# Kernel tuning notes

Measured on AMD Instinct MI355X. Metric: run time of the kernel, lower is better.

Reference implementation:

```python
import jax, jax.numpy as jnp
import numpy as np

N = 150000   # nodes
E = 600000   # edges
F_IN = 32    # node features
H = 128      # hidden_channels == MLP_neurons
G = 2048     # graphs in batch


def setup_inputs() -> dict:
    key = jax.random.key(0)
    ks = iter(jax.random.split(key, 40))
    inp = {}
    inp['x'] = jax.random.normal(next(ks), (N, F_IN), dtype=jnp.float32)
    inp['edge_index'] = jax.random.randint(next(ks), (2, E), 0, N)
    inp['batch'] = jnp.sort(jax.random.randint(next(ks), (N,), 0, G))
    # GINConv MLPs: Linear(in,H) ReLU Linear(H,H) ReLU Linear(H,H)
    for i, f_in in enumerate([F_IN, H, H]):
        s1 = 1.0 / np.sqrt(f_in)
        s2 = 1.0 / np.sqrt(H)
        inp[f'c{i}_w1'] = jax.random.uniform(next(ks), (f_in, H), minval=-s1, maxval=s1)
        inp[f'c{i}_b1'] = jnp.zeros((H,), jnp.float32)
        inp[f'c{i}_w2'] = jax.random.uniform(next(ks), (H, H), minval=-s2, maxval=s2)
        inp[f'c{i}_b2'] = jnp.zeros((H,), jnp.float32)
        inp[f'c{i}_w3'] = jax.random.uniform(next(ks), (H, H), minval=-s2, maxval=s2)
        inp[f'c{i}_b3'] = jnp.zeros((H,), jnp.float32)
    s = 1.0 / np.sqrt(H)
    inp['fc0_w'] = jax.random.uniform(next(ks), (H, H), minval=-s, maxval=s)
    inp['fc0_b'] = jnp.zeros((H,), jnp.float32)
    inp['fc1_w'] = jax.random.uniform(next(ks), (H, H), minval=-s, maxval=s)
    inp['fc1_b'] = jnp.zeros((H,), jnp.float32)
    inp['out_w'] = jax.random.uniform(next(ks), (H, 2), minval=-s, maxval=s)
    inp['out_b'] = jnp.zeros((2,), jnp.float32)
    return inp


def _gin_layer(x, edge_index, w1, b1, w2, b2, w3, b3):
    # GINConv with eps=0: h = MLP(x + sum_{j in N(i)} x_j)
    agg = jax.ops.segment_sum(x[edge_index[0]], edge_index[1], num_segments=N)
    h = x + agg
    h = jax.nn.relu(h @ w1 + b1)
    h = jax.nn.relu(h @ w2 + b2)
    h = h @ w3 + b3
    return jax.nn.relu(h)  # outer .relu() in forward


def reference(x, edge_index, batch,
              c0_w1, c0_b1, c0_w2, c0_b2, c0_w3, c0_b3,
              c1_w1, c1_b1, c1_w2, c1_b2, c1_w3, c1_b3,
              c2_w1, c2_b1, c2_w2, c2_b2, c2_w3, c2_b3,
              fc0_w, fc0_b, fc1_w, fc1_b, out_w, out_b):
    h = _gin_layer(x, edge_index, c0_w1, c0_b1, c0_w2, c0_b2, c0_w3, c0_b3)
    h = _gin_layer(h, edge_index, c1_w1, c1_b1, c1_w2, c1_b2, c1_w3, c1_b3)
    h = _gin_layer(h, edge_index, c2_w1, c2_b1, c2_w2, c2_b2, c2_w3, c2_b3)
    # global_mean_pool over graph ids
    sums = jax.ops.segment_sum(h, batch, num_segments=G)            # [G,H]
    cnts = jax.ops.segment_sum(jnp.ones((N,), h.dtype), batch, num_segments=G)
    g = sums / jnp.maximum(cnts, 1.0)[:, None]
    # classifier head (dropout is identity at inference)
    g = jax.nn.relu(g @ fc0_w + fc0_b)
    g = jax.nn.relu(g @ fc1_w + fc1_b)
    return g @ out_w + out_b  # [G,2]
```

## Files before the change

kernel.cpp:

```cpp
#include <hip/hip_runtime.h>
#include <hip/hip_bf16.h>

#define NN 150000
#define EE 600000
#define F_IN 32
#define HD 128
#define GG 2048
#define CAP 28
#define NP 150016

typedef __attribute__((ext_vector_type(8))) short bf16x8;
typedef __attribute__((ext_vector_type(4))) float f32x4;

__device__ inline void split_bf16(float v, unsigned short& hi, unsigned short& lo) {
    __hip_bfloat16 h = __float2bfloat16(v);
    float hv = __bfloat162float(h);
    __hip_bfloat16 l = __float2bfloat16(v - hv);
    hi = *reinterpret_cast<unsigned short*>(&h);
    lo = *reinterpret_cast<unsigned short*>(&l);
}
__device__ inline unsigned short bf16_hi(float v) {
    __hip_bfloat16 h = __float2bfloat16(v);
    return *reinterpret_cast<unsigned short*>(&h);
}
__device__ inline float bf2f(unsigned short u) {
    union { unsigned int i; float f; } c;
    c.i = ((unsigned int)u) << 16;
    return c.f;
}

__global__ void init_zero(int* __restrict__ cnt_node, float* __restrict__ pooled) {
    int i = blockIdx.x * blockDim.x + threadIdx.x;
    if (i < NN) cnt_node[i] = 0;
    if (i < GG * HD) pooled[i] = 0.f;
}

__global__ void build_graph(const int* __restrict__ ei,
                            int* __restrict__ cnt_node,
                            int* __restrict__ bucket) {
    int e = blockIdx.x * blockDim.x + threadIdx.x;
    if (e >= EE) return;
    int src = ei[e];
    int dst = ei[EE + e];
    int slot = atomicAdd(&cnt_node[dst], 1);
    if (slot < CAP) bucket[dst * CAP + slot] = src;
}

struct PrepDesc { const float* src; unsigned short* dhi; unsigned short* dlo; int K; };
struct PrepArgs { PrepDesc d[9]; };

__global__ void prep_weights(PrepArgs pa) {
    PrepDesc de = pa.d[blockIdx.y];
    int total = de.K * HD;
    int KS = de.K >> 5;
    for (int idx = blockIdx.x * blockDim.x + threadIdx.x; idx < total;
         idx += gridDim.x * blockDim.x) {
        int k = idx / HD, h = idx - (idx / HD) * HD;
        unsigned short hi, lo;
        split_bf16(de.src[idx], hi, lo);
        int nt = h >> 4, m = h & 15;
        int ks = k >> 5, quad = (k >> 3) & 3, e = k & 7;
        int lane = quad * 16 + m;
        int pidx = ((nt * KS + ks) * 64 + lane) * 8 + e;
        de.dhi[pidx] = hi;
        de.dlo[pidx] = lo;
    }
}

template <int K_IN, bool BF16IN, bool POOL>
__launch_bounds__(256, 3)
__global__ void gin_layer(const void* __restrict__ hin_,
                          const int* __restrict__ cnt_node,
                          const int* __restrict__ bucket,
                          const unsigned short* __restrict__ w1h, const unsigned short* __restrict__ w1l,
                          const float* __restrict__ b1,
                          const unsigned short* __restrict__ w2h, const unsigned short* __restrict__ w2l,
                          const float* __restrict__ b2,
                          const unsigned short* __restrict__ w3h, const unsigned short* __restrict__ w3l,
                          const float* __restrict__ b3,
                          unsigned short* __restrict__ out,
                          const int* __restrict__ batch,
                          float* __restrict__ pooled) {
    constexpr int KS1 = K_IN / 32;
    constexpr int UN = BF16IN ? 4 : (KS1 == 1 ? 8 : 2);
    __shared__ unsigned int shp[4][16][128];

    const int wave = threadIdx.x >> 6;
    const int lane = threadIdx.x & 63;
    const int m = lane & 15;
    const int quad = lane >> 4;
    const int nodeBase = blockIdx.x * 128 + wave * 32;

    const float* hf = (const float*)hin_;
    const unsigned short* hb = (const unsigned short*)hin_;

    bf16x8 ah[2][KS1], al[2][KS1];
#pragma unroll
    for (int s = 0; s < 2; s++) {
        int node = nodeBase + s * 16 + m;
        node = node < NN ? node : NN - 1;
        float ag[KS1][8];
        if (BF16IN) {
            const unsigned short* rs = hb + (size_t)node * K_IN + quad * 8;
#pragma unroll
            for (int ks = 0; ks < KS1; ks++) {
                bf16x8 v = *(const bf16x8*)(rs + ks * 32);
#pragma unroll
                for (int e = 0; e < 8; e++) ag[ks][e] = bf2f((unsigned short)v[e]);
            }
        } else {
            const float* rs = hf + (size_t)node * K_IN + quad * 8;
#pragma unroll
            for (int ks = 0; ks < KS1; ks++) {
                float4 v0 = *(const float4*)(rs + ks * 32);
                float4 v1 = *(const float4*)(rs + ks * 32 + 4);
                ag[ks][0] = v0.x; ag[ks][1] = v0.y; ag[ks][2] = v0.z; ag[ks][3] = v0.w;
                ag[ks][4] = v1.x; ag[ks][5] = v1.y; ag[ks][6] = v1.z; ag[ks][7] = v1.w;
            }
        }
        int cnt = cnt_node[node];
        cnt = cnt < CAP ? cnt : CAP;
        const int* b = bucket + (size_t)node * CAP;
        int i = 0;
        if (BF16IN) {
            for (; i + UN <= cnt; i += UN) {
                bf16x8 v[UN][KS1];
#pragma unroll
                for (int j = 0; j < UN; j++) {
                    const unsigned short* r = hb + (size_t)b[i + j] * K_IN + quad * 8;
#pragma unroll
                    for (int ks = 0; ks < KS1; ks++)
                        v[j][ks] = *(const bf16x8*)(r + ks * 32);
                }
#pragma unroll
                for (int ks = 0; ks < KS1; ks++)
#pragma unroll
                    for (int e = 0; e < 8; e++) {
                        float t01 = bf2f((unsigned short)v[0][ks][e]) +
                                    bf2f((unsigned short)v[1][ks][e]);
                        float t23 = bf2f((unsigned short)v[2][ks][e]) +
                                    bf2f((unsigned short)v[3][ks][e]);
                        ag[ks][e] += t01 + t23;
                    }
            }
            for (; i < cnt; i++) {
                const unsigned short* r = hb + (size_t)b[i] * K_IN + quad * 8;
#pragma unroll
                for (int ks = 0; ks < KS1; ks++) {
                    bf16x8 v = *(const bf16x8*)(r + ks * 32);
#pragma unroll
                    for (int e = 0; e < 8; e++) ag[ks][e] += bf2f((unsigned short)v[e]);
                }
            }
        } else {
            for (; i + UN <= cnt; i += UN) {
                float4 v0[UN][KS1], v1[UN][KS1];
#pragma unroll
                for (int j = 0; j < UN; j++) {
                    const float* r = hf + (size_t)b[i + j] * K_IN + quad * 8;
#pragma unroll
                    for (int ks = 0; ks < KS1; ks++) {
                        v0[j][ks] = *(const float4*)(r + ks * 32);
                        v1[j][ks] = *(const float4*)(r + ks * 32 + 4);
                    }
                }
#pragma unroll
                for (int ks = 0; ks < KS1; ks++) {
#pragma unroll
                    for (int e = 0; e < 4; e++) {
                        float s01 = (&v0[0][ks].x)[e] + (&v0[1][ks].x)[e];
                        float s23 = (&v0[2][ks].x)[e] + (&v0[3][ks].x)[e];
                        if (UN == 8) {
                            s01 += (&v0[4][ks].x)[e] + (&v0[5][ks].x)[e];
                            s23 += (&v0[6][ks].x)[e] + (&v0[7][ks].x)[e];
                        }
                        ag[ks][e] += s01 + s23;
                    }
#pragma unroll
                    for (int e = 0; e < 4; e++) {
                        float s01 = (&v1[0][ks].x)[e] + (&v1[1][ks].x)[e];
                        float s23 = (&v1[2][ks].x)[e] + (&v1[3][ks].x)[e];
                        if (UN == 8) {
                            s01 += (&v1[4][ks].x)[e] + (&v1[5][ks].x)[e];
                            s23 += (&v1[6][ks].x)[e] + (&v1[7][ks].x)[e];
                        }
                        ag[ks][e + 4] += s01 + s23;
                    }
                }
            }
            for (; i < cnt; i++) {
                const float* r = hf + (size_t)b[i] * K_IN + quad * 8;
#pragma unroll
                for (int ks = 0; ks < KS1; ks++) {
                    float4 v0 = *(const float4*)(r + ks * 32);
                    float4 v1 = *(const float4*)(r + ks * 32 + 4);
                    ag[ks][0] += v0.x; ag[ks][1] += v0.y; ag[ks][2] += v0.z; ag[ks][3] += v0.w;
                    ag[ks][4] += v1.x; ag[ks][5] += v1.y; ag[ks][6] += v1.z; ag[ks][7] += v1.w;
                }
            }
        }
#pragma unroll
        for (int ks = 0; ks < KS1; ks++) {
            bf16x8 vh, vl;
#pragma unroll
            for (int e = 0; e < 8; e++) {
                unsigned short hi, lo;
                split_bf16(ag[ks][e], hi, lo);
                vh[e] = (short)hi;
                vl[e] = (short)lo;
            }
            ah[s][ks] = vh;
            al[s][ks] = vl;
        }
    }

    bf16x8 a2h[2][4], a2l[2][4];
    const int fxm = (m & 7) << 2;

#pragma unroll
    for (int s = 0; s < 2; s++) {
#pragma unroll 1
        for (int nt = 0; nt < 8; nt++) {
            f32x4 c = {0.f, 0.f, 0.f, 0.f};
#pragma unroll
            for (int ks = 0; ks < KS1; ks++) {
                bf16x8 bh = *(const bf16x8*)(w1h + ((nt * KS1 + ks) * 64 + lane) * 8);
                bf16x8 bl = *(const bf16x8*)(w1l + ((nt * KS1 + ks) * 64 + lane) * 8);
                c = __builtin_amdgcn_mfma_f32_16x16x32_bf16(ah[s][ks], bh, c, 0, 0, 0);
                c = __builtin_amdgcn_mfma_f32_16x16x32_bf16(al[s][ks], bh, c, 0, 0, 0);
                c = __builtin_amdgcn_mfma_f32_16x16x32_bf16(ah[s][ks], bl, c, 0, 0, 0);
            }
            float bj = b1[nt * 16 + m];
#pragma unroll
            for (int r = 0; r < 4; r++) {
                unsigned short hi, lo;
                split_bf16(fmaxf(c[r] + bj, 0.f), hi, lo);
                int row = quad * 4 + r;
                shp[wave][row][(nt * 16 + m) ^ ((row & 7) << 2)] =
                    (unsigned int)hi | ((unsigned int)lo << 16);
            }
        }
#pragma unroll
        for (int ks = 0; ks < 4; ks++) {
            const unsigned int* rowp = &shp[wave][m][0];
            int base = ks * 32 + quad * 8;
            uint4 wa = *(const uint4*)&rowp[base ^ fxm];
            uint4 wb = *(const uint4*)&rowp[(base + 4) ^ fxm];
            union { unsigned int u[4]; bf16x8 v; } ch, cl;
            ch.u[0] = __builtin_amdgcn_perm(wa.y, wa.x, 0x05040100u);
            ch.u[1] = __builtin_amdgcn_perm(wa.w, wa.z, 0x05040100u);
            ch.u[2] = __builtin_amdgcn_perm(wb.y, wb.x, 0x05040100u);
            ch.u[3] = __builtin_amdgcn_perm(wb.w, wb.z, 0x05040100u);
            cl.u[0] = __builtin_amdgcn_perm(wa.y, wa.x, 0x07060302u);
            cl.u[1] = __builtin_amdgcn_perm(wa.w, wa.z, 0x07060302u);
            cl.u[2] = __builtin_amdgcn_perm(wb.y, wb.x, 0x07060302u);
            cl.u[3] = __builtin_amdgcn_perm(wb.w, wb.z, 0x07060302u);
            a2h[s][ks] = ch.v;
            a2l[s][ks] = cl.v;
        }
    }

#pragma unroll
    for (int s = 0; s < 2; s++) {
#pragma unroll 1
        for (int nt = 0; nt < 8; nt++) {
            f32x4 c = {0.f, 0.f, 0.f, 0.f};
#pragma unroll
            for (int ks = 0; ks < 4; ks++) {
                bf16x8 bh = *(const bf16x8*)(w2h + ((nt * 4 + ks) * 64 + lane) * 8);
                bf16x8 bl = *(const bf16x8*)(w2l + ((nt * 4 + ks) * 64 + lane) * 8);
                c = __builtin_amdgcn_mfma_f32_16x16x32_bf16(a2h[s][ks], bh, c, 0, 0, 0);
                c = __builtin_amdgcn_mfma_f32_16x16x32_bf16(a2l[s][ks], bh, c, 0, 0, 0);
                c = __builtin_amdgcn_mfma_f32_16x16x32_bf16(a2h[s][ks], bl, c, 0, 0, 0);
            }
            float bj = b2[nt * 16 + m];
#pragma unroll
            for (int r = 0; r < 4; r++) {
                unsigned short hi, lo;
                split_bf16(fmaxf(c[r] + bj, 0.f), hi, lo);
                int row = quad * 4 + r;
                shp[wave][row][(nt * 16 + m) ^ ((row & 7) << 2)] =
                    (unsigned int)hi | ((unsigned int)lo << 16);
            }
        }
#pragma unroll
        for (int ks = 0; ks < 4; ks++) {
            const unsigned int* rowp = &shp[wave][m][0];
            int base = ks * 32 + quad * 8;
            uint4 wa = *(const uint4*)&rowp[base ^ fxm];
            uint4 wb = *(const uint4*)&rowp[(base + 4) ^ fxm];
            union { unsigned int u[4]; bf16x8 v; } ch, cl;
            ch.u[0] = __builtin_amdgcn_perm(wa.y, wa.x, 0x05040100u);
            ch.u[1] = __builtin_amdgcn_perm(wa.w, wa.z, 0x05040100u);
            ch.u[2] = __builtin_amdgcn_perm(wb.y, wb.x, 0x05040100u);
            ch.u[3] = __builtin_amdgcn_perm(wb.w, wb.z, 0x05040100u);
            cl.u[0] = __builtin_amdgcn_perm(wa.y, wa.x, 0x07060302u);
            cl.u[1] = __builtin_amdgcn_perm(wa.w, wa.z, 0x07060302u);
            cl.u[2] = __builtin_amdgcn_perm(wb.y, wb.x, 0x07060302u);
            cl.u[3] = __builtin_amdgcn_perm(wb.w, wb.z, 0x07060302u);
            a2h[s][ks] = ch.v;
            a2l[s][ks] = cl.v;
        }
    }

    if (POOL) {
        float* shf = (float*)&shp[wave][0][0];
#pragma unroll
        for (int h = 0; h < 2; h++) {
#pragma unroll 1
            for (int nt = 0; nt < 8; nt++) {
                f32x4 c = {0.f, 0.f, 0.f, 0.f};
#pragma unroll
                for (int ks = 0; ks < 4; ks++) {
                    bf16x8 bh = *(const bf16x8*)(w3h + ((nt * 4 + ks) * 64 + lane) * 8);
                    bf16x8 bl = *(const bf16x8*)(w3l + ((nt * 4 + ks) * 64 + lane) * 8);
                    c = __builtin_amdgcn_mfma_f32_16x16x32_bf16(a2h[h][ks], bh, c, 0, 0, 0);
                    c = __builtin_amdgcn_mfma_f32_16x16x32_bf16(a2l[h][ks], bh, c, 0, 0, 0);
                    c = __builtin_amdgcn_mfma_f32_16x16x32_bf16(a2h[h][ks], bl, c, 0, 0, 0);
                }
                float bj = b3[nt * 16 + m];
#pragma unroll
                for (int r = 0; r < 4; r++) {
                    int row = quad * 4 + r;
                    shf[row * 128 + ((nt * 16 + m) ^ ((row & 7) << 2))] =
                        fmaxf(c[r] + bj, 0.f);
                }
            }
            int c0 = lane * 2;
            float run0 = 0.f, run1 = 0.f;
            int gp = -1;
            for (int rrow = 0; rrow < 16; rrow++) {
                int node = nodeBase + h * 16 + rrow;
                if (node >= NN) break;
                int g = batch[node];
                float2 xv = *(const float2*)&shf[rrow * 128 + (c0 ^ ((rrow & 7) << 2))];
                if (g != gp) {
                    if (gp >= 0) {
                        atomicAdd(&pooled[(size_t)gp * HD + c0 + 0], run0);
                        atomicAdd(&pooled[(size_t)gp * HD + c0 + 1], run1);
                    }
                    run0 = xv.x; run1 = xv.y; gp = g;
                } else {
                    run0 += xv.x; run1 += xv.y;
                }
            }
            if (gp >= 0) {
                atomicAdd(&pooled[(size_t)gp * HD + c0 + 0], run0);
                atomicAdd(&pooled[(size_t)gp * HD + c0 + 1], run1);
            }
        }
    } else {
        unsigned short* sh16 = (unsigned short*)&shp[wave][0][0];
#pragma unroll
        for (int s = 0; s < 2; s++) {
#pragma unroll 1
            for (int nt = 0; nt < 8; nt++) {
                f32x4 c = {0.f, 0.f, 0.f, 0.f};
#pragma unroll
                for (int ks = 0; ks < 4; ks++) {
                    bf16x8 bh = *(const bf16x8*)(w3h + ((nt * 4 + ks) * 64 + lane) * 8);
                    bf16x8 bl = *(const bf16x8*)(w3l + ((nt * 4 + ks) * 64 + lane) * 8);
                    c = __builtin_amdgcn_mfma_f32_16x16x32_bf16(a2h[s][ks], bh, c, 0, 0, 0);
                    c = __builtin_amdgcn_mfma_f32_16x16x32_bf16(a2l[s][ks], bh, c, 0, 0, 0);
                    c = __builtin_amdgcn_mfma_f32_16x16x32_bf16(a2h[s][ks], bl, c, 0, 0, 0);
                }
                float bj = b3[nt * 16 + m];
#pragma unroll
                for (int r = 0; r < 4; r++) {
                    int row = quad * 4 + r;
                    int hh = nt * 16 + m;
                    int w2 = (hh >> 1) ^ ((row & 7) << 2);
                    sh16[row * 256 + w2 * 2 + (hh & 1)] =
                        bf16_hi(fmaxf(c[r] + bj, 0.f));
                }
            }
#pragma unroll
            for (int io = 0; io < 4; io++) {
                int row16 = io * 4 + quad;
                int wbase = (m * 4) ^ ((row16 & 7) << 2);
                int n2 = nodeBase + s * 16 + row16;
                bf16x8 v = *(const bf16x8*)&sh16[row16 * 256 + wbase * 2];
                if (n2 < NN) *(bf16x8*)&out[(size_t)n2 * HD + m * 8] = v;
            }
        }
    }
}

__device__ inline int lb_batch(const int* __restrict__ batch, int key) {
    int lo = 0, hi = NN;
    while (lo < hi) {
        int mid = (lo + hi) >> 1;
        if (batch[mid] < key) lo = mid + 1; else hi = mid;
    }
    return lo;
}

__launch_bounds__(128)
__global__ void head(const float* __restrict__ pooled, const int* __restrict__ batch,
                     const float* __restrict__ fc0_w, const float* __restrict__ fc0_b,
                     const float* __restrict__ fc1_w, const float* __restrict__ fc1_b,
                     const float* __restrict__ out_w, const float* __restrict__ out_b,
                     float* __restrict__ out) {
    int g = blockIdx.x;
    int j = threadIdx.x;
    __shared__ float s0[HD];
    __shared__ float s1[HD];
    int c = lb_batch(batch, g + 1) - lb_batch(batch, g);
    float cf = (float)(c > 1 ? c : 1);
    s0[j] = pooled[(size_t)g * HD + j] / cf;
    __syncthreads();

    float acc = fc0_b[j];
    for (int k = 0; k < HD; k += 4) {
        float4 hv = *(const float4*)&s0[k];
        acc = fmaf(hv.x, fc0_w[(k + 0) * HD + j], acc);
        acc = fmaf(hv.y, fc0_w[(k + 1) * HD + j], acc);
        acc = fmaf(hv.z, fc0_w[(k + 2) * HD + j], acc);
        acc = fmaf(hv.w, fc0_w[(k + 3) * HD + j], acc);
    }
    s1[j] = fmaxf(acc, 0.0f);
    __syncthreads();

    acc = fc1_b[j];
    for (int k = 0; k < HD; k += 4) {
        float4 hv = *(const float4*)&s1[k];
        acc = fmaf(hv.x, fc1_w[(k + 0) * HD + j], acc);
        acc = fmaf(hv.y, fc1_w[(k + 1) * HD + j], acc);
        acc = fmaf(hv.z, fc1_w[(k + 2) * HD + j], acc);
        acc = fmaf(hv.w, fc1_w[(k + 3) * HD + j], acc);
    }
    float v = fmaxf(acc, 0.0f);

    float p0 = v * out_w[j * 2 + 0];
    float p1 = v * out_w[j * 2 + 1];
    __syncthreads();
    s0[j] = p0;
    s1[j] = p1;
    __syncthreads();
    for (int off = 64; off >= 1; off >>= 1) {
        if (j < off) {
            s0[j] += s0[j + off];
            s1[j] += s1[j + off];
        }
        __syncthreads();
    }
    if (j == 0) {
        out[(size_t)g * 2 + 0] = s0[0] + out_b[0];
        out[(size_t)g * 2 + 1] = s1[0] + out_b[1];
    }
}

extern "C" void kernel_launch(void* const* d_in, const int* in_sizes, int n_in,
                              void* d_out, int out_size, void* d_ws, size_t ws_size,
                              hipStream_t stream) {
    const float* x     = (const float*)d_in[0];
    const int*   ei    = (const int*)d_in[1];
    const int*   batch = (const int*)d_in[2];
    const float* cw[3][6];
    for (int i = 0; i < 3; i++)
        for (int k = 0; k < 6; k++) cw[i][k] = (const float*)d_in[3 + 6 * i + k];
    const float* fc0_w = (const float*)d_in[21];
    const float* fc0_b = (const float*)d_in[22];
    const float* fc1_w = (const float*)d_in[23];
    const float* fc1_b = (const float*)d_in[24];
    const float* out_w = (const float*)d_in[25];
    const float* out_b = (const float*)d_in[26];
    float* out = (float*)d_out;

    char* ws = (char*)d_ws;
    size_t off = 0;
    auto carve = [&](size_t bytes) {
        void* p = ws + off;
        off += (bytes + 255) & ~(size_t)255;
        return p;
    };
    int*   cnt_node = (int*)carve((size_t)NN * 4);
    float* pooled   = (float*)carve((size_t)GG * HD * 4);
    int*   bucket   = (int*)carve((size_t)NN * CAP * 4);
    unsigned short* hA = (unsigned short*)carve((size_t)NP * HD * 2);
    unsigned short* hB = (unsigned short*)carve((size_t)NP * HD * 2);
    unsigned short* wHi[9];
    unsigned short* wLo[9];
    int wK[9] = {F_IN, HD, HD, HD, HD, HD, HD, HD, HD};
    for (int i = 0; i < 9; i++) {
        wHi[i] = (unsigned short*)carve((size_t)wK[i] * HD * 2);
        wLo[i] = (unsigned short*)carve((size_t)wK[i] * HD * 2);
    }
    (void)ws_size;

    init_zero<<<(GG * HD + 255) / 256, 256, 0, stream>>>(cnt_node, pooled);
    build_graph<<<(EE + 255) / 256, 256, 0, stream>>>(ei, cnt_node, bucket);

    PrepArgs pa;
    for (int l = 0; l < 3; l++)
        for (int s = 0; s < 3; s++) {
            int i = l * 3 + s;
            pa.d[i].src = cw[l][2 * s];
            pa.d[i].dhi = wHi[i];
            pa.d[i].dlo = wLo[i];
            pa.d[i].K = wK[i];
        }
    prep_weights<<<dim3(16, 9), 256, 0, stream>>>(pa);

    const int blocks = NP / 128;

    gin_layer<F_IN, false, false><<<blocks, 256, 0, stream>>>(x, cnt_node, bucket,
        wHi[0], wLo[0], cw[0][1], wHi[1], wLo[1], cw[0][3], wHi[2], wLo[2], cw[0][5],
        hA, batch, pooled);
    gin_layer<HD, true, false><<<blocks, 256, 0, stream>>>(hA, cnt_node, bucket,
        wHi[3], wLo[3], cw[1][1], wHi[4], wLo[4], cw[1][3], wHi[5], wLo[5], cw[1][5],
        hB, batch, pooled);
    gin_layer<HD, true, true><<<blocks, 256, 0, stream>>>(hB, cnt_node, bucket,
        wHi[6], wLo[6], cw[2][1], wHi[7], wLo[7], cw[2][3], wHi[8], wLo[8], cw[2][5],
        nullptr, batch, pooled);

    head<<<GG, 128, 0, stream>>>(pooled, batch, fc0_w, fc0_b, fc1_w, fc1_b, out_w, out_b, out);
}
```

Baseline: 459.9 us.

## Prefetch next weight tile in MFMA loops and predicate neighbor gather with vector index loads

Each of the three MLP GEMM loops now loads the weight fragments for the next output tile one iteration ahead, so global weight-load latency overlaps the current tile's MFMAs. The neighbor gather loops are replaced by a single 4-wide loop that reads four bucket indices at once with a vector load, masks out-of-range slots, and drops the scalar tail loop. Node and neighbor feature reads become nontemporal loads. This raises register pressure and may lower occupancy under the 256x3 launch bounds. The nontemporal hints may also hurt cache reuse of neighbor rows that are read repeatedly.

```diff
diff --git a/kernel.cpp b/kernel.cpp
--- a/kernel.cpp
+++ b/kernel.cpp
@@ -11,6 +11,7 @@
 
 typedef __attribute__((ext_vector_type(8))) short bf16x8;
 typedef __attribute__((ext_vector_type(4))) float f32x4;
+typedef __attribute__((ext_vector_type(4))) int i32x4;
 
 __device__ inline void split_bf16(float v, unsigned short& hi, unsigned short& lo) {
     __hip_bfloat16 h = __float2bfloat16(v);
@@ -82,7 +83,6 @@
                           const int* __restrict__ batch,
                           float* __restrict__ pooled) {
     constexpr int KS1 = K_IN / 32;
-    constexpr int UN = BF16IN ? 4 : (KS1 == 1 ? 8 : 2);
     __shared__ unsigned int shp[4][16][128];
 
     const int wave = threadIdx.x >> 6;
@@ -104,98 +104,88 @@
             const unsigned short* rs = hb + (size_t)node * K_IN + quad * 8;
 #pragma unroll
             for (int ks = 0; ks < KS1; ks++) {
-                bf16x8 v = *(const bf16x8*)(rs + ks * 32);
+                bf16x8 v = __builtin_nontemporal_load((const bf16x8*)(rs + ks * 32));
 #pragma unroll
                 for (int e = 0; e < 8; e++) ag[ks][e] = bf2f((unsigned short)v[e]);
             }
         } else {
             const float* rs = hf + (size_t)node * K_IN + quad * 8;
-#pragma unroll
-            for (int ks = 0; ks < KS1; ks++) {
-                float4 v0 = *(const float4*)(rs + ks * 32);
-                float4 v1 = *(const float4*)(rs + ks * 32 + 4);
-                ag[ks][0] = v0.x; ag[ks][1] = v0.y; ag[ks][2] = v0.z; ag[ks][3] = v0.w;
-                ag[ks][4] = v1.x; ag[ks][5] = v1.y; ag[ks][6] = v1.z; ag[ks][7] = v1.w;
-            }
+            f32x4 v0 = __builtin_nontemporal_load((const f32x4*)rs);
+            f32x4 v1 = __builtin_nontemporal_load((const f32x4*)(rs + 4));
+#pragma unroll
+            for (int e = 0; e < 4; e++) { ag[0][e] = v0[e]; ag[0][e + 4] = v1[e]; }
         }
         int cnt = cnt_node[node];
         cnt = cnt < CAP ? cnt : CAP;
         const int* b = bucket + (size_t)node * CAP;
-        int i = 0;
         if (BF16IN) {
-            for (; i + UN <= cnt; i += UN) {
-                bf16x8 v[UN][KS1];
-#pragma unroll
-                for (int j = 0; j < UN; j++) {
-                    const unsigned short* r = hb + (size_t)b[i + j] * K_IN + quad * 8;
-#pragma unroll
-                    for (int ks = 0; ks < KS1; ks++)
-                        v[j][ks] = *(const bf16x8*)(r + ks * 32);
+#pragma unroll 1
+            for (int i = 0; i < cnt; i += 4) {
+                i32x4 iv = __builtin_nontemporal_load((const i32x4*)(b + i));
+                bool k1 = i + 1 < cnt, k2 = i + 2 < cnt, k3 = i + 3 < cnt;
+                int j0 = iv[0];
+                int j1 = k1 ? iv[1] : j0;
+                int j2 = k2 ? iv[2] : j0;
+                int j3 = k3 ? iv[3] : j0;
+                bf16x8 v0[KS1], v1[KS1], v2[KS1], v3[KS1];
+                const unsigned short* r0 = hb + (size_t)j0 * K_IN + quad * 8;
+                const unsigned short* r1 = hb + (size_t)j1 * K_IN + quad * 8;
+                const unsigned short* r2 = hb + (size_t)j2 * K_IN + quad * 8;
+                const unsigned short* r3 = hb + (size_t)j3 * K_IN + quad * 8;
+#pragma unroll
+                for (int ks = 0; ks < KS1; ks++) {
+                    v0[ks] = __builtin_nontemporal_load((const bf16x8*)(r0 + ks * 32));
+                    v1[ks] = __builtin_nontemporal_load((const bf16x8*)(r1 + ks * 32));
+                    v2[ks] = __builtin_nontemporal_load((const bf16x8*)(r2 + ks * 32));
+                    v3[ks] = __builtin_nontemporal_load((const bf16x8*)(r3 + ks * 32));
                 }
 #pragma unroll
                 for (int ks = 0; ks < KS1; ks++)
 #pragma unroll
                     for (int e = 0; e < 8; e++) {
-                        float t01 = bf2f((unsigned short)v[0][ks][e]) +
-                                    bf2f((unsigned short)v[1][ks][e]);
-                        float t23 = bf2f((unsigned short)v[2][ks][e]) +
-                                    bf2f((unsigned short)v[3][ks][e]);
-                        ag[ks][e] += t01 + t23;
+                        float t0 = bf2f((unsigned short)v0[ks][e]);
+                        float t1 = bf2f((unsigned short)v1[ks][e]); t1 = k1 ? t1 : 0.f;
+                        float t2 = bf2f((unsigned short)v2[ks][e]); t2 = k2 ? t2 : 0.f;
+                        float t3 = bf2f((unsigned short)v3[ks][e]); t3 = k3 ? t3 : 0.f;
+                        ag[ks][e] += (t0 + t1) + (t2 + t3);
                     }
             }
-            for (; i < cnt; i++) {
-                const unsigned short* r = hb + (size_t)b[i] * K_IN + quad * 8;
-#pragma unroll
-                for (int ks = 0; ks < KS1; ks++) {
-                    bf16x8 v = *(const bf16x8*)(r + ks * 32);
-#pragma unroll
-                    for (int e = 0; e < 8; e++) ag[ks][e] += bf2f((unsigned short)v[e]);
-                }
-            }
         } else {
-            for (; i + UN <= cnt; i += UN) {
-                float4 v0[UN][KS1], v1[UN][KS1];
-#pragma unroll
-                for (int j = 0; j < UN; j++) {
-                    const float* r = hf + (size_t)b[i + j] * K_IN + quad * 8;
-#pragma unroll
-                    for (int ks = 0; ks < KS1; ks++) {
-                        v0[j][ks] = *(const float4*)(r + ks * 32);
-                        v1[j][ks] = *(const float4*)(r + ks * 32 + 4);
-                    }
-                }
-#pragma unroll
-                for (int ks = 0; ks < KS1; ks++) {
-#pragma unroll
-                    for (int e = 0; e < 4; e++) {
-                        float s01 = (&v0[0][ks].x)[e] + (&v0[1][ks].x)[e];
-                        float s23 = (&v0[2][ks].x)[e] + (&v0[3][ks].x)[e];
-                        if (UN == 8) {
-                            s01 += (&v0[4][ks].x)[e] + (&v0[5][ks].x)[e];
-                            s23 += (&v0[6][ks].x)[e] + (&v0[7][ks].x)[e];
-                        }
-                        ag[ks][e] += s01 + s23;
-                    }
-#pragma unroll
-                    for (int e = 0; e < 4; e++) {
-                        float s01 = (&v1[0][ks].x)[e] + (&v1[1][ks].x)[e];
-                        float s23 = (&v1[2][ks].x)[e] + (&v1[3][ks].x)[e];
-                        if (UN == 8) {
-                            s01 += (&v1[4][ks].x)[e] + (&v1[5][ks].x)[e];
-                            s23 += (&v1[6][ks].x)[e] + (&v1[7][ks].x)[e];
-                        }
-                        ag[ks][e + 4] += s01 + s23;
-                    }
-                }
-            }
-            for (; i < cnt; i++) {
-                const float* r = hf + (size_t)b[i] * K_IN + quad * 8;
-#pragma unroll
-                for (int ks = 0; ks < KS1; ks++) {
-                    float4 v0 = *(const float4*)(r + ks * 32);
-                    float4 v1 = *(const float4*)(r + ks * 32 + 4);
-                    ag[ks][0] += v0.x; ag[ks][1] += v0.y; ag[ks][2] += v0.z; ag[ks][3] += v0.w;
-                    ag[ks][4] += v1.x; ag[ks][5] += v1.y; ag[ks][6] += v1.z; ag[ks][7] += v1.w;
+#pragma unroll 1
+            for (int i = 0; i < cnt; i += 4) {
+                i32x4 iv = __builtin_nontemporal_load((const i32x4*)(b + i));
+                bool k1 = i + 1 < cnt, k2 = i + 2 < cnt, k3 = i + 3 < cnt;
+                int j0 = iv[0];
+                int j1 = k1 ? iv[1] : j0;
+                int j2 = k2 ? iv[2] : j0;
+                int j3 = k3 ? iv[3] : j0;
+                const float* r0 = hf + (size_t)j0 * K_IN + quad * 8;
+                const float* r1 = hf + (size_t)j1 * K_IN + quad * 8;
+                const float* r2 = hf + (size_t)j2 * K_IN + quad * 8;
+                const float* r3 = hf + (size_t)j3 * K_IN + quad * 8;
+                f32x4 a0 = __builtin_nontemporal_load((const f32x4*)r0);
+                f32x4 b0 = __builtin_nontemporal_load((const f32x4*)(r0 + 4));
+                f32x4 a1 = __builtin_nontemporal_load((const f32x4*)r1);
+                f32x4 b1v = __builtin_nontemporal_load((const f32x4*)(r1 + 4));
+                f32x4 a2 = __builtin_nontemporal_load((const f32x4*)r2);
+                f32x4 b2v = __builtin_nontemporal_load((const f32x4*)(r2 + 4));
+                f32x4 a3 = __builtin_nontemporal_load((const f32x4*)r3);
+                f32x4 b3v = __builtin_nontemporal_load((const f32x4*)(r3 + 4));
+#pragma unroll
+                for (int e = 0; e < 4; e++) {
+                    float t0 = a0[e];
+                    float t1 = k1 ? a1[e] : 0.f;
+                    float t2 = k2 ? a2[e] : 0.f;
+                    float t3 = k3 ? a3[e] : 0.f;
+                    ag[0][e] += (t0 + t1) + (t2 + t3);
+                }
+#pragma unroll
+                for (int e = 0; e < 4; e++) {
+                    float t0 = b0[e];
+                    float t1 = k1 ? b1v[e] : 0.f;
+                    float t2 = k2 ? b2v[e] : 0.f;
+                    float t3 = k3 ? b3v[e] : 0.f;
+                    ag[0][e + 4] += (t0 + t1) + (t2 + t3);
                 }
             }
         }
@@ -219,16 +209,27 @@
 
 #pragma unroll
     for (int s = 0; s < 2; s++) {
-#pragma unroll 1
+        bf16x8 bhc[KS1], blc[KS1];
+#pragma unroll
+        for (int ks = 0; ks < KS1; ks++) {
+            bhc[ks] = *(const bf16x8*)(w1h + (ks * 64 + lane) * 8);
+            blc[ks] = *(const bf16x8*)(w1l + (ks * 64 + lane) * 8);
+        }
+#pragma unroll 2
         for (int nt = 0; nt < 8; nt++) {
+            int ntn = (nt + 1) & 7;
+            bf16x8 bhn[KS1], bln[KS1];
+#pragma unroll
+            for (int ks = 0; ks < KS1; ks++) {
+                bhn[ks] = *(const bf16x8*)(w1h + ((ntn * KS1 + ks) * 64 + lane) * 8);
+                bln[ks] = *(const bf16x8*)(w1l + ((ntn * KS1 + ks) * 64 + lane) * 8);
+            }
             f32x4 c = {0.f, 0.f, 0.f, 0.f};
 #pragma unroll
             for (int ks = 0; ks < KS1; ks++) {
-                bf16x8 bh = *(const bf16x8*)(w1h + ((nt * KS1 + ks) * 64 + lane) * 8);
-                bf16x8 bl = *(const bf16x8*)(w1l + ((nt * KS1 + ks) * 64 + lane) * 8);
-                c = __builtin_amdgcn_mfma_f32_16x16x32_bf16(ah[s][ks], bh, c, 0, 0, 0);
-                c = __builtin_amdgcn_mfma_f32_16x16x32_bf16(al[s][ks], bh, c, 0, 0, 0);
-                c = __builtin_amdgcn_mfma_f32_16x16x32_bf16(ah[s][ks], bl, c, 0, 0, 0);
+                c = __builtin_amdgcn_mfma_f32_16x16x32_bf16(ah[s][ks], bhc[ks], c, 0, 0, 0);
+                c = __builtin_amdgcn_mfma_f32_16x16x32_bf16(al[s][ks], bhc[ks], c, 0, 0, 0);
+                c = __builtin_amdgcn_mfma_f32_16x16x32_bf16(ah[s][ks], blc[ks], c, 0, 0, 0);
             }
             float bj = b1[nt * 16 + m];
 #pragma unroll
@@ -239,6 +240,8 @@
                 shp[wave][row][(nt * 16 + m) ^ ((row & 7) << 2)] =
                     (unsigned int)hi | ((unsigned int)lo << 16);
             }
+#pragma unroll
+            for (int ks = 0; ks < KS1; ks++) { bhc[ks] = bhn[ks]; blc[ks] = bln[ks]; }
         }
 #pragma unroll
         for (int ks = 0; ks < 4; ks++) {
@@ -262,16 +265,27 @@
 
 #pragma unroll
     for (int s = 0; s < 2; s++) {
-#pragma unroll 1
+        bf16x8 bhc[4], blc[4];
+#pragma unroll
+        for (int ks = 0; ks < 4; ks++) {
+            bhc[ks] = *(const bf16x8*)(w2h + (ks * 64 + lane) * 8);
+            blc[ks] = *(const bf16x8*)(w2l + (ks * 64 + lane) * 8);
+        }
+#pragma unroll 2
         for (int nt = 0; nt < 8; nt++) {
+            int ntn = (nt + 1) & 7;
+            bf16x8 bhn[4], bln[4];
+#pragma unroll
+            for (int ks = 0; ks < 4; ks++) {
+                bhn[ks] = *(const bf16x8*)(w2h + ((ntn * 4 + ks) * 64 + lane) * 8);
+                bln[ks] = *(const bf16x8*)(w2l + ((ntn * 4 + ks) * 64 + lane) * 8);
+            }
             f32x4 c = {0.f, 0.f, 0.f, 0.f};
 #pragma unroll
             for (int ks = 0; ks < 4; ks++) {
-                bf16x8 bh = *(const bf16x8*)(w2h + ((nt * 4 + ks) * 64 + lane) * 8);
-                bf16x8 bl = *(const bf16x8*)(w2l + ((nt * 4 + ks) * 64 + lane) * 8);
-                c = __builtin_amdgcn_mfma_f32_16x16x32_bf16(a2h[s][ks], bh, c, 0, 0, 0);
-                c = __builtin_amdgcn_mfma_f32_16x16x32_bf16(a2l[s][ks], bh, c, 0, 0, 0);
-                c = __builtin_amdgcn_mfma_f32_16x16x32_bf16(a2h[s][ks], bl, c, 0, 0, 0);
+                c = __builtin_amdgcn_mfma_f32_16x16x32_bf16(a2h[s][ks], bhc[ks], c, 0, 0, 0);
+                c = __builtin_amdgcn_mfma_f32_16x16x32_bf16(a2l[s][ks], bhc[ks], c, 0, 0, 0);
+                c = __builtin_amdgcn_mfma_f32_16x16x32_bf16(a2h[s][ks], blc[ks], c, 0, 0, 0);
             }
             float bj = b2[nt * 16 + m];
 #pragma unroll
@@ -282,6 +296,8 @@
                 shp[wave][row][(nt * 16 + m) ^ ((row & 7) << 2)] =
                     (unsigned int)hi | ((unsigned int)lo << 16);
             }
+#pragma unroll
+            for (int ks = 0; ks < 4; ks++) { bhc[ks] = bhn[ks]; blc[ks] = bln[ks]; }
         }
 #pragma unroll
         for (int ks = 0; ks < 4; ks++) {
@@ -306,17 +322,28 @@
     if (POOL) {
         float* shf = (float*)&shp[wave][0][0];
 #pragma unroll
-        for (int h = 0; h < 2; h++) {
-#pragma unroll 1
+        for (int s = 0; s < 2; s++) {
+            bf16x8 bhc[4], blc[4];
+#pragma unroll
+            for (int ks = 0; ks < 4; ks++) {
+                bhc[ks] = *(const bf16x8*)(w3h + (ks * 64 + lane) * 8);
+                blc[ks] = *(const bf16x8*)(w3l + (ks * 64 + lane) * 8);
+            }
+#pragma unroll 2
             for (int nt = 0; nt < 8; nt++) {
+                int ntn = (nt + 1) & 7;
+                bf16x8 bhn[4], bln[4];
+#pragma unroll
+                for (int ks = 0; ks < 4; ks++) {
+                    bhn[ks] = *(const bf16x8*)(w3h + ((ntn * 4 + ks) * 64 + lane) * 8);
+                    bln[ks] = *(const bf16x8*)(w3l + ((ntn * 4 + ks) * 64 + lane) * 8);
+                }
                 f32x4 c = {0.f, 0.f, 0.f, 0.f};
 #pragma unroll
                 for (int ks = 0; ks < 4; ks++) {
-                    bf16x8 bh = *(const bf16x8*)(w3h + ((nt * 4 + ks) * 64 + lane) * 8);
-                    bf16x8 bl = *(const bf16x8*)(w3l + ((nt * 4 + ks) * 64 + lane) * 8);
-                    c = __builtin_amdgcn_mfma_f32_16x16x32_bf16(a2h[h][ks], bh, c, 0, 0, 0);
-                    c = __builtin_amdgcn_mfma_f32_16x16x32_bf16(a2l[h][ks], bh, c, 0, 0, 0);
-                    c = __builtin_amdgcn_mfma_f32_16x16x32_bf16(a2h[h][ks], bl, c, 0, 0, 0);
+                    c = __builtin_amdgcn_mfma_f32_16x16x32_bf16(a2h[s][ks], bhc[ks], c, 0, 0, 0);
+                    c = __builtin_amdgcn_mfma_f32_16x16x32_bf16(a2l[s][ks], bhc[ks], c, 0, 0, 0);
+                    c = __builtin_amdgcn_mfma_f32_16x16x32_bf16(a2h[s][ks], blc[ks], c, 0, 0, 0);
                 }
                 float bj = b3[nt * 16 + m];
 #pragma unroll
@@ -325,12 +352,14 @@
                     shf[row * 128 + ((nt * 16 + m) ^ ((row & 7) << 2))] =
                         fmaxf(c[r] + bj, 0.f);
                 }
+#pragma unroll
+                for (int ks = 0; ks < 4; ks++) { bhc[ks] = bhn[ks]; blc[ks] = bln[ks]; }
             }
             int c0 = lane * 2;
             float run0 = 0.f, run1 = 0.f;
             int gp = -1;
             for (int rrow = 0; rrow < 16; rrow++) {
-                int node = nodeBase + h * 16 + rrow;
+                int node = nodeBase + s * 16 + rrow;
                 if (node >= NN) break;
                 int g = batch[node];
                 float2 xv = *(const float2*)&shf[rrow * 128 + (c0 ^ ((rrow & 7) << 2))];
@@ -353,16 +382,27 @@
         unsigned short* sh16 = (unsigned short*)&shp[wave][0][0];
 #pragma unroll
         for (int s = 0; s < 2; s++) {
-#pragma unroll 1
+            bf16x8 bhc[4], blc[4];
+#pragma unroll
+            for (int ks = 0; ks < 4; ks++) {
+                bhc[ks] = *(const bf16x8*)(w3h + (ks * 64 + lane) * 8);
+                blc[ks] = *(const bf16x8*)(w3l + (ks * 64 + lane) * 8);
+            }
+#pragma unroll 2
             for (int nt = 0; nt < 8; nt++) {
+                int ntn = (nt + 1) & 7;
+                bf16x8 bhn[4], bln[4];
+#pragma unroll
+                for (int ks = 0; ks < 4; ks++) {
+                    bhn[ks] = *(const bf16x8*)(w3h + ((ntn * 4 + ks) * 64 + lane) * 8);
+                    bln[ks] = *(const bf16x8*)(w3l + ((ntn * 4 + ks) * 64 + lane) * 8);
+                }
                 f32x4 c = {0.f, 0.f, 0.f, 0.f};
 #pragma unroll
                 for (int ks = 0; ks < 4; ks++) {
-                    bf16x8 bh = *(const bf16x8*)(w3h + ((nt * 4 + ks) * 64 + lane) * 8);
-                    bf16x8 bl = *(const bf16x8*)(w3l + ((nt * 4 + ks) * 64 + lane) * 8);
-                    c = __builtin_amdgcn_mfma_f32_16x16x32_bf16(a2h[s][ks], bh, c, 0, 0, 0);
-                    c = __builtin_amdgcn_mfma_f32_16x16x32_bf16(a2l[s][ks], bh, c, 0, 0, 0);
-                    c = __builtin_amdgcn_mfma_f32_16x16x32_bf16(a2h[s][ks], bl, c, 0, 0, 0);
+                    c = __builtin_amdgcn_mfma_f32_16x16x32_bf16(a2h[s][ks], bhc[ks], c, 0, 0, 0);
+                    c = __builtin_amdgcn_mfma_f32_16x16x32_bf16(a2l[s][ks], bhc[ks], c, 0, 0, 0);
+                    c = __builtin_amdgcn_mfma_f32_16x16x32_bf16(a2h[s][ks], blc[ks], c, 0, 0, 0);
                 }
                 float bj = b3[nt * 16 + m];
 #pragma unroll
@@ -373,6 +413,8 @@
                     sh16[row * 256 + w2 * 2 + (hh & 1)] =
                         bf16_hi(fmaxf(c[r] + bj, 0.f));
                 }
+#pragma unroll
+                for (int ks = 0; ks < 4; ks++) { bhc[ks] = bhn[ks]; blc[ks] = bln[ks]; }
             }
 #pragma unroll
             for (int io = 0; io < 4; io++) {
```

Result: slower. 508.7 us (+10.6%).
